# Kernel optimization log

Hardware: AMD Instinct MI355X
Metric: run time of the kernel (lower is better)

## Reference

```python
import jax, jax.numpy as jnp
import numpy as np

N, IN, H, M, D = 2048, 400, 256, 128, 8


def setup_inputs() -> dict:
    key = jax.random.key(0)
    ks = jax.random.split(key, 20)
    g = lambda k, shp, s: jax.random.normal(k, shp, jnp.float32) * s
    C = IN // 2
    return {
        "x": g(ks[0], (N, IN), 1.0),
        "memory": g(ks[1], (N, H, M), 1.0),
        "ke_w": g(ks[2], (H, C), 1.0 / np.sqrt(C)),
        "ke_b": g(ks[3], (H,), 0.01),
        "km_w": g(ks[4], (M, H), 1.0 / np.sqrt(H)),
        "km_b": g(ks[5], (M,), 0.01),
        "kw2_w": g(ks[6], (D, H), 1.0 / np.sqrt(H)),
        "kw2_b": g(ks[7], (D,), 0.01),
        "sum_w": g(ks[8], (H, 2 * H), 1.0 / np.sqrt(2 * H)),
        "sum_b": g(ks[9], (H,), 0.01),
        "out_w": g(ks[10], (1, H), 1.0 / np.sqrt(H)),
        "out_b": g(ks[11], (1,), 0.01),
        "ve_w": g(ks[12], (H, IN), 1.0 / np.sqrt(IN)),
        "ve_b": g(ks[13], (H,), 0.01),
        "er_w": g(ks[14], (D, H, H), 1.0 / np.sqrt(H)),
        "er_b": g(ks[15], (D, H), 0.01),
        "ad_w": g(ks[16], (D, H, H), 1.0 / np.sqrt(H)),
        "ad_b": g(ks[17], (D, H), 0.01),
    }


def reference(x, memory, ke_w, ke_b, km_w, km_b, kw2_w, kw2_b,
              sum_w, sum_b, out_w, out_b, ve_w, ve_b,
              er_w, er_b, ad_w, ad_b):
    n, c2 = x.shape
    c = c2 // 2
    # query = sum of the two halves of x
    q = x.reshape(n, 2, c).sum(axis=1)                       # (N, C)
    k = q @ ke_w.T + ke_b                                    # (N, H)
    w = jax.nn.softmax(k @ km_w.T + km_b, axis=-1)           # (N, M) read/write weights
    w2 = jax.nn.softmax(k @ kw2_w.T + kw2_b, axis=-1)        # (N, D) expert gates
    # memory read: weighted sum over memory slots
    r = jnp.einsum('nhm,nm->nh', memory, w)                  # (N, H)
    f = jnp.tanh(jnp.concatenate([k, r], axis=1) @ sum_w.T + sum_b)
    y = f @ out_w.T + out_b                                  # (N, 1)
    v = x @ ve_w.T + ve_b                                    # (N, H)
    # DynamicLinear: gate-weighted mixture of per-expert linear maps
    # (fused: avoids materializing per-sample (N,H,H) weights)
    e = jax.nn.sigmoid(jnp.einsum('ni,doi,nd->no', v, er_w, w2) + w2 @ er_b)
    a = jnp.tanh(jnp.einsum('ni,doi,nd->no', v, ad_w, w2) + w2 @ ad_b)
    # memory write: erase then add
    memory = memory * (1.0 - w[:, None, :] * e[:, :, None])
    memory = memory + w[:, None, :] * a[:, :, None]
    return y, memory
```

## Files before the change

### kernel.cpp

```cpp
#include <hip/hip_runtime.h>
#include <math.h>

#define N_  2048
#define IN_ 400
#define C_  200
#define H_  256
#define M_  128
#define D_  8

#define KQ   224
#define KX   416
#define KBIG 2112
#define NZ   6
#define KSPL (KBIG / NZ)
#define KS   512

typedef __bf16 bf16x8 __attribute__((ext_vector_type(8)));
typedef float  f32x4  __attribute__((ext_vector_type(4)));

__device__ __forceinline__ ushort f2bf(float x) { __bf16 b = (__bf16)x; return __builtin_bit_cast(ushort, b); }
__device__ __forceinline__ float  bf2f(ushort u) { unsigned v = ((unsigned)u) << 16; return __builtin_bit_cast(float, v); }

__device__ __forceinline__ float4 f4z() { return make_float4(0.f, 0.f, 0.f, 0.f); }
__device__ __forceinline__ float4 ld4p(const float* p, bool v) { return v ? *(const float4*)p : f4z(); }
__device__ __forceinline__ float4 add4(float4 a, float4 b) {
    return make_float4(a.x + b.x, a.y + b.y, a.z + b.z, a.w + b.w);
}
__device__ __forceinline__ uint4 pack8(float4 a, float4 b) {
    ushort u[8] = { f2bf(a.x), f2bf(a.y), f2bf(a.z), f2bf(a.w),
                    f2bf(b.x), f2bf(b.y), f2bf(b.z), f2bf(b.w) };
    return *(uint4*)u;
}

template<class F>
__device__ __forceinline__ void gemm_core(
    F&& ld, const float* __restrict__ bias,
    void* __restrict__ Cv, int ldc, int outbf,
    int m0, int n0, int kFrom, int kTo,
    ushort (*As)[128][40], ushort (*Bs)[64][40])
{
    const int tid = threadIdx.x, lane = tid & 63, wave = tid >> 6;
    const int wm = (wave >> 1) * 64, wn = (wave & 1) * 32;
    const int sr = tid >> 2, sc = (tid & 3) * 8;

    f32x4 acc[4][2] = {};

    auto compute = [&](int b) {
        const int ko = (lane >> 4) * 8;
        bf16x8 af[4], bfr[2];
#pragma unroll
        for (int i = 0; i < 4; i++)
            af[i] = __builtin_bit_cast(bf16x8, *(const uint4*)&As[b][wm + i * 16 + (lane & 15)][ko]);
#pragma unroll
        for (int j = 0; j < 2; j++)
            bfr[j] = __builtin_bit_cast(bf16x8, *(const uint4*)&Bs[b][wn + j * 16 + (lane & 15)][ko]);
#pragma unroll
        for (int i = 0; i < 4; i++)
#pragma unroll
            for (int j = 0; j < 2; j++)
                acc[i][j] = __builtin_amdgcn_mfma_f32_16x16x32_bf16(af[i], bfr[j], acc[i][j], 0, 0, 0);
    };

    uint4 a0, a1, b0;
    ld(kFrom, a0, a1, b0);
    *(uint4*)&As[0][sr][sc] = a0;
    *(uint4*)&As[0][sr + 64][sc] = a1;
    *(uint4*)&Bs[0][sr][sc] = b0;
    __syncthreads();

    int cur = 0;
    for (int k0 = kFrom + 32; k0 < kTo; k0 += 32) {
        ld(k0, a0, a1, b0);
        compute(cur);
        *(uint4*)&As[cur ^ 1][sr][sc] = a0;
        *(uint4*)&As[cur ^ 1][sr + 64][sc] = a1;
        *(uint4*)&Bs[cur ^ 1][sr][sc] = b0;
        __syncthreads();
        cur ^= 1;
    }
    compute(cur);

    float* Cf = (float*)Cv;
    ushort* Cb = (ushort*)Cv;
#pragma unroll
    for (int i = 0; i < 4; i++) {
#pragma unroll
        for (int j = 0; j < 2; j++) {
            int row = m0 + wm + i * 16 + (lane >> 4) * 4;
            int col = n0 + wn + j * 16 + (lane & 15);
#pragma unroll
            for (int r = 0; r < 4; r++) {
                float val = acc[i][j][r];
                if (bias) val += bias[col];
                if (outbf) Cb[(size_t)(row + r) * ldc + col] = f2bf(val);
                else       Cf[(size_t)(row + r) * ldc + col] = val;
            }
        }
    }
}

__global__ __launch_bounds__(256) void k1_kernel(
    const float* __restrict__ x,
    const float* __restrict__ ke_w, const float* __restrict__ ke_b, ushort* __restrict__ kr,
    const float* __restrict__ ve_w, const float* __restrict__ ve_b, float* __restrict__ v,
    const float* __restrict__ er_w, const float* __restrict__ er_b,
    const float* __restrict__ ad_w, const float* __restrict__ ad_b,
    ushort* __restrict__ wcat)
{
    __shared__ ushort As[2][128][40];
    __shared__ ushort Bs[2][64][40];
    const int z = blockIdx.z;
    const int sr = threadIdx.x >> 2, sc = (threadIdx.x & 3) * 8;

    if (z == 0) {
        const int m0 = blockIdx.y * 128, n0 = blockIdx.x * 64;
        auto ld = [&](int k0, uint4& A0, uint4& A1, uint4& B0) {
            int c0 = k0 + sc, c4 = c0 + 4;
            bool v0 = c0 < C_, v4 = c4 < C_;
            const float* r0 = x + (size_t)(m0 + sr) * IN_;
            const float* r1 = x + (size_t)(m0 + sr + 64) * IN_;
            A0 = pack8(add4(ld4p(r0 + c0, v0), ld4p(r0 + C_ + c0, v0)),
                       add4(ld4p(r0 + c4, v4), ld4p(r0 + C_ + c4, v4)));
            A1 = pack8(add4(ld4p(r1 + c0, v0), ld4p(r1 + C_ + c0, v0)),
                       add4(ld4p(r1 + c4, v4), ld4p(r1 + C_ + c4, v4)));
            const float* rb = ke_w + (size_t)(n0 + sr) * C_;
            B0 = pack8(ld4p(rb + c0, v0), ld4p(rb + c4, v4));
        };
        gemm_core(ld, ke_b, kr, KS, 1, m0, n0, 0, KQ, As, Bs);
    } else if (z == 1) {
        const int m0 = blockIdx.y * 128, n0 = blockIdx.x * 64;
        auto ld = [&](int k0, uint4& A0, uint4& A1, uint4& B0) {
            int c0 = k0 + sc, c4 = c0 + 4;
            bool v0 = c0 < IN_, v4 = c4 < IN_;
            const float* r0 = x + (size_t)(m0 + sr) * IN_;
            const float* r1 = x + (size_t)(m0 + sr + 64) * IN_;
            A0 = pack8(ld4p(r0 + c0, v0), ld4p(r0 + c4, v4));
            A1 = pack8(ld4p(r1 + c0, v0), ld4p(r1 + c4, v4));
            const float* rb = ve_w + (size_t)(n0 + sr) * IN_;
            B0 = pack8(ld4p(rb + c0, v0), ld4p(rb + c4, v4));
        };
        gemm_core(ld, ve_b, v, H_, 0, m0, n0, 0, KX, As, Bs);
    } else {
        int idx = ((z - 2) * 64 + blockIdx.y * 4 + blockIdx.x) * 256 + threadIdx.x;
        if (idx >= 512 * (KBIG / 4)) return;
        int oc = idx / (KBIG / 4), g = idx % (KBIG / 4), c0 = g * 4;
        const float* Wsrc = (oc < 256) ? er_w : ad_w;
        const float* bsrc = (oc < 256) ? er_b : ad_b;
        int oo = oc & 255;
        ushort pk[4];
#pragma unroll
        for (int j = 0; j < 4; j++) {
            int c = c0 + j;
            float val = 0.f;
            if (c < 2048)      { int d = c >> 8, ii = c & 255; val = Wsrc[(size_t)(d * 256 + oo) * 256 + ii]; }
            else if (c < 2056) { val = bsrc[(c - 2048) * 256 + oo]; }
            pk[j] = f2bf(val);
        }
        *(ushort4*)&wcat[(size_t)oc * KBIG + c0] = *(ushort4*)pk;
    }
}

__global__ __launch_bounds__(256) void vww_kernel(
    const ushort* __restrict__ kr, const float* __restrict__ v,
    const float* __restrict__ kw2_w, const float* __restrict__ kw2_b,
    const float* __restrict__ km_w, const float* __restrict__ km_b,
    float* __restrict__ wlog, ushort* __restrict__ vw)
{
    __shared__ ushort As[2][128][40];
    __shared__ ushort Bs[2][64][40];
    __shared__ float kf[H_], vl[H_], lg[8], w2l[8];
    const int b = blockIdx.x, t = threadIdx.x;
    const int sr = t >> 2, sc = (t & 3) * 8;

    if (b < 32) {
        const int m0 = (b >> 1) * 128, n0 = (b & 1) * 64;
        auto ld = [&](int k0, uint4& A0, uint4& A1, uint4& B0) {
            A0 = *(const uint4*)&kr[(size_t)(m0 + sr) * KS + k0 + sc];
            A1 = *(const uint4*)&kr[(size_t)(m0 + sr + 64) * KS + k0 + sc];
            int c0 = k0 + sc, c4 = c0 + 4;
            const float* rb = km_w + (size_t)(n0 + sr) * H_;
            B0 = pack8(*(const float4*)(rb + c0), *(const float4*)(rb + c4));
        };
        gemm_core(ld, km_b, wlog, M_, 0, m0, n0, 0, H_, As, Bs);
        return;
    }

    const int n = b - 32;
    if (t < 64) {
        ushort4 u = ((const ushort4*)(kr + (size_t)n * KS))[t];
        kf[t * 4 + 0] = bf2f(u.x); kf[t * 4 + 1] = bf2f(u.y);
        kf[t * 4 + 2] = bf2f(u.z); kf[t * 4 + 3] = bf2f(u.w);
        float4 vv = ((const float4*)(v + (size_t)n * H_))[t];
        vl[t * 4 + 0] = vv.x; vl[t * 4 + 1] = vv.y;
        vl[t * 4 + 2] = vv.z; vl[t * 4 + 3] = vv.w;
    }
    __syncthreads();
    {
        int d = t >> 5, l = t & 31;
        float acc = 0.f;
        const float* wr = kw2_w + d * H_;
#pragma unroll
        for (int s = 0; s < 8; s++) acc += kf[l + 32 * s] * wr[l + 32 * s];
#pragma unroll
        for (int off = 16; off; off >>= 1) acc += __shfl_xor(acc, off);
        if (l == 0) lg[d] = acc + kw2_b[d];
    }
    __syncthreads();
    if (t < 8) {
        float val = lg[t];
        float mx = val;
#pragma unroll
        for (int off = 1; off < 8; off <<= 1) mx = fmaxf(mx, __shfl_xor(mx, off));
        float e = expf(val - mx), s = e;
#pragma unroll
        for (int off = 1; off < 8; off <<= 1) s += __shfl_xor(s, off);
        w2l[t] = e / s;
    }
    __syncthreads();
    ushort* row = vw + (size_t)n * KBIG;
    for (int g = t; g < KBIG / 4; g += 256) {
        int c0 = g * 4;
        ushort pk[4];
#pragma unroll
        for (int j = 0; j < 4; j++) {
            int c = c0 + j;
            float val = 0.f;
            if (c < 2048)      val = w2l[c >> 8] * vl[c & 255];
            else if (c < 2056) val = w2l[c - 2048];
            pk[j] = f2bf(val);
        }
        *(ushort4*)&row[c0] = *(ushort4*)pk;
    }
}

__global__ __launch_bounds__(256) void bigw_kernel(
    const ushort* __restrict__ vw, const ushort* __restrict__ Wcat,
    float* __restrict__ parts)
{
    __shared__ ushort As[2][128][40];
    __shared__ ushort Bs[2][64][40];
    const int z = blockIdx.z;
    const int m0 = blockIdx.y * 128, n0 = blockIdx.x * 64;
    const int sr = threadIdx.x >> 2, sc = (threadIdx.x & 3) * 8;
    auto ld = [&](int k0, uint4& A0, uint4& A1, uint4& B0) {
        A0 = *(const uint4*)&vw[(size_t)(m0 + sr) * KBIG + k0 + sc];
        A1 = *(const uint4*)&vw[(size_t)(m0 + sr + 64) * KBIG + k0 + sc];
        B0 = *(const uint4*)&Wcat[(size_t)(n0 + sr) * KBIG + k0 + sc];
    };
    gemm_core(ld, nullptr, parts + (size_t)z * N_ * 512, 512, 0,
              m0, n0, z * KSPL, (z + 1) * KSPL, As, Bs);
}

__global__ __launch_bounds__(256) void mem_stream_kernel(
    const float* __restrict__ mem_in,
    const float* __restrict__ wlog,
    const float* __restrict__ parts,
    float* __restrict__ mem_out,
    ushort* __restrict__ kr)
{
    __shared__ float wl[M_];
    __shared__ float el[128], al[128];
    __shared__ float red[4];
    const int n = blockIdx.x >> 1, half = blockIdx.x & 1, hbase = half * 128;
    const int t = threadIdx.x;

    const int col = (t < 128) ? (hbase + t) : (256 + hbase + (t - 128));
    float pacc = 0.f;
#pragma unroll
    for (int z = 0; z < NZ; z++)
        pacc += parts[(size_t)z * N_ * 512 + (size_t)n * 512 + col];

    float lv = 0.f;
    if (t < 128) {
        lv = wlog[(size_t)n * M_ + t];
        float mx = lv;
#pragma unroll
        for (int off = 32; off; off >>= 1) mx = fmaxf(mx, __shfl_xor(mx, off));
        if ((t & 63) == 0) red[t >> 6] = mx;
        el[t] = 1.f / (1.f + expf(-pacc));
    } else {
        al[t - 128] = tanhf(pacc);
    }
    __syncthreads();
    if (t < 128) {
        float gmax = fmaxf(red[0], red[1]);
        float ev = expf(lv - gmax);
        float s = ev;
#pragma unroll
        for (int off = 32; off; off >>= 1) s += __shfl_xor(s, off);
        if ((t & 63) == 0) red[2 + (t >> 6)] = s;
        wl[t] = ev;
    }
    __syncthreads();
    if (t < 128) wl[t] *= 1.f / (red[2] + red[3]);
    __syncthreads();

    const int wave = t >> 6, lane = t & 63, half2 = lane >> 5, l32 = lane & 31;
    const int hrow = wave * 2 + half2;
    const f32x4* min4 = (const f32x4*)(mem_in + ((size_t)n * H_ + hbase) * M_);
    f32x4* mout4 = (f32x4*)(mem_out + ((size_t)n * H_ + hbase) * M_);
    f32x4 wv = ((const f32x4*)wl)[l32];

    float racc[16];
    float eh[16], ah[16];
#pragma unroll
    for (int i = 0; i < 16; i++) { eh[i] = el[i * 8 + hrow]; ah[i] = al[i * 8 + hrow]; }
#pragma unroll
    for (int i = 0; i < 16; i++) {
        f32x4 mv = __builtin_nontemporal_load(&min4[(i * 8 + hrow) * 32 + l32]);
        f32x4 nv = mv * (1.f - wv * eh[i]) + wv * ah[i];
        __builtin_nontemporal_store(nv, &mout4[(i * 8 + hrow) * 32 + l32]);
        racc[i] = mv[0] * wv[0] + mv[1] * wv[1] + mv[2] * wv[2] + mv[3] * wv[3];
    }

#pragma unroll
    for (int i = 0; i < 16; i++) {
        float r = racc[i];
#pragma unroll
        for (int off = 1; off < 32; off <<= 1) r += __shfl_xor(r, off);
        if (l32 == 0) kr[(size_t)n * KS + H_ + hbase + i * 8 + hrow] = f2bf(r);
    }
}

__global__ __launch_bounds__(256) void fy_kernel(
    const ushort* __restrict__ kr, const float* __restrict__ sum_w,
    const float* __restrict__ sum_b, const float* __restrict__ out_w,
    const float* __restrict__ out_b, float* __restrict__ y)
{
    __shared__ ushort As[2][64][40];
    __shared__ ushort Bs[2][256][40];
    __shared__ float yl[64][4];
    const int tid = threadIdx.x, lane = tid & 63, wave = tid >> 6;
    const int wn = wave * 64;
    const int m0 = blockIdx.x * 64;
    const int sr = tid >> 2, sc = (tid & 3) * 8;

    f32x4 acc[4][4] = {};

    auto compute = [&](int b) {
        const int ko = (lane >> 4) * 8;
        bf16x8 af[4], bfr[4];
#pragma unroll
        for (int i = 0; i < 4; i++)
            af[i] = __builtin_bit_cast(bf16x8, *(const uint4*)&As[b][i * 16 + (lane & 15)][ko]);
#pragma unroll
        for (int j = 0; j < 4; j++)
            bfr[j] = __builtin_bit_cast(bf16x8, *(const uint4*)&Bs[b][wn + j * 16 + (lane & 15)][ko]);
#pragma unroll
        for (int i = 0; i < 4; i++)
#pragma unroll
            for (int j = 0; j < 4; j++)
                acc[i][j] = __builtin_amdgcn_mfma_f32_16x16x32_bf16(af[i], bfr[j], acc[i][j], 0, 0, 0);
    };

    auto stage = [&](int buf, int k0) {
        int c0 = k0 + sc, c4 = c0 + 4;
        *(uint4*)&As[buf][sr][sc] = *(const uint4*)&kr[(size_t)(m0 + sr) * KS + k0 + sc];
#pragma unroll
        for (int g = 0; g < 4; g++) {
            const float* rb = sum_w + (size_t)(sr + g * 64) * KS;
            *(uint4*)&Bs[buf][sr + g * 64][sc] = pack8(*(const float4*)(rb + c0), *(const float4*)(rb + c4));
        }
    };

    stage(0, 0);
    __syncthreads();
    int cur = 0;
    for (int k0 = 32; k0 < KS; k0 += 32) {
        compute(cur);
        stage(cur ^ 1, k0);
        __syncthreads();
        cur ^= 1;
    }
    compute(cur);

    float ow[4], sb[4];
#pragma unroll
    for (int j = 0; j < 4; j++) {
        int col = wn + j * 16 + (lane & 15);
        ow[j] = out_w[col];
        sb[j] = sum_b[col];
    }
    float yp[4][4];
#pragma unroll
    for (int i = 0; i < 4; i++)
#pragma unroll
        for (int r = 0; r < 4; r++) {
            float s = 0.f;
#pragma unroll
            for (int j = 0; j < 4; j++)
                s += tanhf(acc[i][j][r] + sb[j]) * ow[j];
            yp[i][r] = s;
        }
#pragma unroll
    for (int off = 1; off < 16; off <<= 1)
#pragma unroll
        for (int i = 0; i < 4; i++)
#pragma unroll
            for (int r = 0; r < 4; r++)
                yp[i][r] += __shfl_xor(yp[i][r], off);
    if ((lane & 15) == 0) {
#pragma unroll
        for (int i = 0; i < 4; i++)
#pragma unroll
            for (int r = 0; r < 4; r++)
                yl[i * 16 + (lane >> 4) * 4 + r][wave] = yp[i][r];
    }
    __syncthreads();
    if (tid < 64)
        y[m0 + tid] = yl[tid][0] + yl[tid][1] + yl[tid][2] + yl[tid][3] + out_b[0];
}

extern "C" void kernel_launch(void* const* d_in, const int* in_sizes, int n_in,
                              void* d_out, int out_size, void* d_ws, size_t ws_size,
                              hipStream_t stream) {
    const float* x      = (const float*)d_in[0];
    const float* mem_in = (const float*)d_in[1];
    const float* ke_w   = (const float*)d_in[2];
    const float* ke_b   = (const float*)d_in[3];
    const float* km_w   = (const float*)d_in[4];
    const float* km_b   = (const float*)d_in[5];
    const float* kw2_w  = (const float*)d_in[6];
    const float* kw2_b  = (const float*)d_in[7];
    const float* sum_w  = (const float*)d_in[8];
    const float* sum_b  = (const float*)d_in[9];
    const float* out_w  = (const float*)d_in[10];
    const float* out_b  = (const float*)d_in[11];
    const float* ve_w   = (const float*)d_in[12];
    const float* ve_b   = (const float*)d_in[13];
    const float* er_w   = (const float*)d_in[14];
    const float* er_b   = (const float*)d_in[15];
    const float* ad_w   = (const float*)d_in[16];
    const float* ad_b   = (const float*)d_in[17];

    float* y_out   = (float*)d_out;
    float* mem_out = (float*)d_out + N_;

    float* ws = (float*)d_ws;
    size_t o = 0;
    float*  parts = ws + o;            o += (size_t)NZ * N_ * 512;
    ushort* vw    = (ushort*)(ws + o); o += (size_t)N_ * KBIG / 2;
    ushort* Wcat  = (ushort*)(ws + o); o += (size_t)512 * KBIG / 2;
    ushort* kr    = (ushort*)(ws + o); o += (size_t)N_ * KS / 2;
    float*  v     = ws + o;            o += (size_t)N_ * H_;
    float*  wlog  = ws + o;            o += (size_t)N_ * M_;

    k1_kernel<<<dim3(4, 16, 19), 256, 0, stream>>>(
        x, ke_w, ke_b, kr, ve_w, ve_b, v, er_w, er_b, ad_w, ad_b, Wcat);
    vww_kernel<<<32 + N_, 256, 0, stream>>>(
        kr, v, kw2_w, kw2_b, km_w, km_b, wlog, vw);
    bigw_kernel<<<dim3(8, 16, NZ), 256, 0, stream>>>(vw, Wcat, parts);
    mem_stream_kernel<<<2 * N_, 256, 0, stream>>>(mem_in, wlog, parts, mem_out, kr);
    fy_kernel<<<N_ / 64, 256, 0, stream>>>(kr, sum_w, sum_b, out_w, out_b, y_out);
}
```

Measured before the change: 174.6 us.

## Restructure memory stream kernel to two samples per block with software-pipelined loads

```diff
diff --git a/kernel.cpp b/kernel.cpp
--- a/kernel.cpp
+++ b/kernel.cpp
@@ -258,67 +258,87 @@
     float* __restrict__ mem_out,
     ushort* __restrict__ kr)
 {
-    __shared__ float wl[M_];
-    __shared__ float el[128], al[128];
-    __shared__ float red[4];
-    const int n = blockIdx.x >> 1, half = blockIdx.x & 1, hbase = half * 128;
+    __shared__ float wl2[2][M_];
+    __shared__ float el2[2][H_], al2[2][H_];
+    __shared__ float red[2][4];
+    const int n0 = blockIdx.x * 2;
     const int t = threadIdx.x;
 
-    const int col = (t < 128) ? (hbase + t) : (256 + hbase + (t - 128));
-    float pacc = 0.f;
-#pragma unroll
-    for (int z = 0; z < NZ; z++)
-        pacc += parts[(size_t)z * N_ * 512 + (size_t)n * 512 + col];
-
-    float lv = 0.f;
-    if (t < 128) {
-        lv = wlog[(size_t)n * M_ + t];
+#pragma unroll
+    for (int it = 0; it < 4; it++) {
+        int idx = it * 256 + t;
+        int rep = idx >> 9, cc = idx & 511;
+        float pacc = 0.f;
+#pragma unroll
+        for (int z = 0; z < NZ; z++)
+            pacc += parts[(size_t)z * N_ * 512 + (size_t)(n0 + rep) * 512 + cc];
+        if (cc < 256) el2[rep][cc] = 1.f / (1.f + expf(-pacc));
+        else          al2[rep][cc - 256] = tanhf(pacc);
+    }
+
+    {
+        const int pair = t >> 7, tp = t & 127, wip = (t >> 6) & 1;
+        float lv = wlog[(size_t)(n0 + pair) * M_ + tp];
         float mx = lv;
 #pragma unroll
         for (int off = 32; off; off >>= 1) mx = fmaxf(mx, __shfl_xor(mx, off));
-        if ((t & 63) == 0) red[t >> 6] = mx;
-        el[t] = 1.f / (1.f + expf(-pacc));
-    } else {
-        al[t - 128] = tanhf(pacc);
-    }
-    __syncthreads();
-    if (t < 128) {
-        float gmax = fmaxf(red[0], red[1]);
+        if ((t & 63) == 0) red[pair][wip] = mx;
+        __syncthreads();
+        float gmax = fmaxf(red[pair][0], red[pair][1]);
         float ev = expf(lv - gmax);
         float s = ev;
 #pragma unroll
         for (int off = 32; off; off >>= 1) s += __shfl_xor(s, off);
-        if ((t & 63) == 0) red[2 + (t >> 6)] = s;
-        wl[t] = ev;
-    }
-    __syncthreads();
-    if (t < 128) wl[t] *= 1.f / (red[2] + red[3]);
+        if ((t & 63) == 0) red[pair][2 + wip] = s;
+        __syncthreads();
+        wl2[pair][tp] = ev / (red[pair][2] + red[pair][3]);
+    }
     __syncthreads();
 
     const int wave = t >> 6, lane = t & 63, half2 = lane >> 5, l32 = lane & 31;
     const int hrow = wave * 2 + half2;
-    const f32x4* min4 = (const f32x4*)(mem_in + ((size_t)n * H_ + hbase) * M_);
-    f32x4* mout4 = (f32x4*)(mem_out + ((size_t)n * H_ + hbase) * M_);
-    f32x4 wv = ((const f32x4*)wl)[l32];
-
-    float racc[16];
-    float eh[16], ah[16];
-#pragma unroll
-    for (int i = 0; i < 16; i++) { eh[i] = el[i * 8 + hrow]; ah[i] = al[i * 8 + hrow]; }
-#pragma unroll
-    for (int i = 0; i < 16; i++) {
-        f32x4 mv = __builtin_nontemporal_load(&min4[(i * 8 + hrow) * 32 + l32]);
-        f32x4 nv = mv * (1.f - wv * eh[i]) + wv * ah[i];
-        __builtin_nontemporal_store(nv, &mout4[(i * 8 + hrow) * 32 + l32]);
-        racc[i] = mv[0] * wv[0] + mv[1] * wv[1] + mv[2] * wv[2] + mv[3] * wv[3];
-    }
-
-#pragma unroll
-    for (int i = 0; i < 16; i++) {
-        float r = racc[i];
-#pragma unroll
-        for (int off = 1; off < 32; off <<= 1) r += __shfl_xor(r, off);
-        if (l32 == 0) kr[(size_t)n * KS + H_ + hbase + i * 8 + hrow] = f2bf(r);
+
+#pragma unroll
+    for (int rep = 0; rep < 2; rep++) {
+        const int n = n0 + rep;
+        const f32x4* min4 = (const f32x4*)(mem_in + (size_t)n * H_ * M_);
+        f32x4* mout4 = (f32x4*)(mem_out + (size_t)n * H_ * M_);
+        f32x4 wv = ((const f32x4*)wl2[rep])[l32];
+
+        f32x4 mv[2][4];
+#pragma unroll
+        for (int j = 0; j < 4; j++)
+            mv[0][j] = __builtin_nontemporal_load(&min4[(j * 8 + hrow) * 32 + l32]);
+
+#pragma unroll
+        for (int c = 0; c < 8; c++) {
+            if (c < 7) {
+#pragma unroll
+                for (int j = 0; j < 4; j++)
+                    mv[(c + 1) & 1][j] = __builtin_nontemporal_load(
+                        &min4[(((c + 1) * 4 + j) * 8 + hrow) * 32 + l32]);
+            }
+            __builtin_amdgcn_sched_barrier(0);
+            float racc[4];
+#pragma unroll
+            for (int j = 0; j < 4; j++) {
+                int row = (c * 4 + j) * 8 + hrow;
+                f32x4 m = mv[c & 1][j];
+                float eh = el2[rep][row], ah = al2[rep][row];
+                f32x4 nv = m * (1.f - wv * eh) + wv * ah;
+                mout4[row * 32 + l32] = nv;
+                racc[j] = m[0] * wv[0] + m[1] * wv[1] + m[2] * wv[2] + m[3] * wv[3];
+            }
+#pragma unroll
+            for (int j = 0; j < 4; j++) {
+                float r = racc[j];
+#pragma unroll
+                for (int off = 1; off < 32; off <<= 1) r += __shfl_xor(r, off);
+                if (l32 == 0)
+                    kr[(size_t)n * KS + H_ + (c * 4 + j) * 8 + hrow] = f2bf(r);
+            }
+            __builtin_amdgcn_sched_barrier(0);
+        }
     }
 }
 
@@ -450,6 +470,6 @@
     vww_kernel<<<32 + N_, 256, 0, stream>>>(
         kr, v, kw2_w, kw2_b, km_w, km_b, wlog, vw);
     bigw_kernel<<<dim3(8, 16, NZ), 256, 0, stream>>>(vw, Wcat, parts);
-    mem_stream_kernel<<<2 * N_, 256, 0, stream>>>(mem_in, wlog, parts, mem_out, kr);
+    mem_stream_kernel<<<N_ / 2, 256, 0, stream>>>(mem_in, wlog, parts, mem_out, kr);
     fy_kernel<<<N_ / 64, 256, 0, stream>>>(kr, sum_w, sum_b, out_w, out_b, y_out);
 }
```

After: 175.1 us. No clear change (+0.3%).

## Stream memory tiles through LDS with async global_load_lds in quarter-row blocks

Applied to the files above, without the earlier changes.

```diff
diff --git a/kernel.cpp b/kernel.cpp
--- a/kernel.cpp
+++ b/kernel.cpp
@@ -17,6 +17,9 @@
 
 typedef __bf16 bf16x8 __attribute__((ext_vector_type(8)));
 typedef float  f32x4  __attribute__((ext_vector_type(4)));
+
+typedef const __attribute__((address_space(1))) unsigned int* gas_t;
+typedef __attribute__((address_space(3))) unsigned int* las_t;
 
 __device__ __forceinline__ ushort f2bf(float x) { __bf16 b = (__bf16)x; return __builtin_bit_cast(ushort, b); }
 __device__ __forceinline__ float  bf2f(ushort u) { unsigned v = ((unsigned)u) << 16; return __builtin_bit_cast(float, v); }
@@ -258,67 +261,82 @@
     float* __restrict__ mem_out,
     ushort* __restrict__ kr)
 {
+    __shared__ float ring[4][2048];
     __shared__ float wl[M_];
-    __shared__ float el[128], al[128];
+    __shared__ float el[64], al[64];
     __shared__ float red[4];
-    const int n = blockIdx.x >> 1, half = blockIdx.x & 1, hbase = half * 128;
+    const int n = blockIdx.x >> 2, q = blockIdx.x & 3, hbase = q * 64;
     const int t = threadIdx.x;
-
-    const int col = (t < 128) ? (hbase + t) : (256 + hbase + (t - 128));
-    float pacc = 0.f;
-#pragma unroll
-    for (int z = 0; z < NZ; z++)
-        pacc += parts[(size_t)z * N_ * 512 + (size_t)n * 512 + col];
 
     float lv = 0.f;
     if (t < 128) {
-        lv = wlog[(size_t)n * M_ + t];
+        int isA = t >> 6, tt = t & 63;
+        int col = isA * 256 + hbase + tt;
+        float pacc = 0.f;
+#pragma unroll
+        for (int z = 0; z < NZ; z++)
+            pacc += parts[(size_t)z * N_ * 512 + (size_t)n * 512 + col];
+        if (isA) al[tt] = tanhf(pacc);
+        else     el[tt] = 1.f / (1.f + expf(-pacc));
+    } else {
+        int tt = t - 128;
+        lv = wlog[(size_t)n * M_ + tt];
         float mx = lv;
 #pragma unroll
         for (int off = 32; off; off >>= 1) mx = fmaxf(mx, __shfl_xor(mx, off));
-        if ((t & 63) == 0) red[t >> 6] = mx;
-        el[t] = 1.f / (1.f + expf(-pacc));
-    } else {
-        al[t - 128] = tanhf(pacc);
-    }
-    __syncthreads();
-    if (t < 128) {
+        if ((t & 63) == 0) red[(t >> 6) - 2] = mx;
+    }
+    __syncthreads();
+    if (t >= 128) {
+        int tt = t - 128;
         float gmax = fmaxf(red[0], red[1]);
         float ev = expf(lv - gmax);
         float s = ev;
 #pragma unroll
         for (int off = 32; off; off >>= 1) s += __shfl_xor(s, off);
-        if ((t & 63) == 0) red[2 + (t >> 6)] = s;
-        wl[t] = ev;
-    }
-    __syncthreads();
-    if (t < 128) wl[t] *= 1.f / (red[2] + red[3]);
-    __syncthreads();
-
-    const int wave = t >> 6, lane = t & 63, half2 = lane >> 5, l32 = lane & 31;
-    const int hrow = wave * 2 + half2;
-    const f32x4* min4 = (const f32x4*)(mem_in + ((size_t)n * H_ + hbase) * M_);
-    f32x4* mout4 = (f32x4*)(mem_out + ((size_t)n * H_ + hbase) * M_);
+        if ((t & 63) == 0) red[2 + (t >> 6) - 2] = s;
+        wl[tt] = ev;
+    }
+    __syncthreads();
+    if (t >= 128) wl[t - 128] *= 1.f / (red[2] + red[3]);
+    __syncthreads();
+
+    const int wave = t >> 6, lane = t & 63;
+    const int l32 = lane & 31, hi = lane >> 5;
+    const int rowg0 = hbase + wave * 16;
+    const float* gsrc = mem_in + ((size_t)n * H_ + rowg0) * M_;
+    float* gdst = mem_out + ((size_t)n * H_ + rowg0) * M_;
+    float* lbase = ring[wave];
+
+#pragma unroll
+    for (int c = 0; c < 8; c++) {
+        __builtin_amdgcn_global_load_lds(
+            (gas_t)(const void*)(gsrc + c * 256 + lane * 4),
+            (las_t)(void*)(lbase + c * 256),
+            16, 0, 0);
+    }
+
     f32x4 wv = ((const f32x4*)wl)[l32];
-
-    float racc[16];
-    float eh[16], ah[16];
-#pragma unroll
-    for (int i = 0; i < 16; i++) { eh[i] = el[i * 8 + hrow]; ah[i] = al[i * 8 + hrow]; }
-#pragma unroll
-    for (int i = 0; i < 16; i++) {
-        f32x4 mv = __builtin_nontemporal_load(&min4[(i * 8 + hrow) * 32 + l32]);
-        f32x4 nv = mv * (1.f - wv * eh[i]) + wv * ah[i];
-        __builtin_nontemporal_store(nv, &mout4[(i * 8 + hrow) * 32 + l32]);
-        racc[i] = mv[0] * wv[0] + mv[1] * wv[1] + mv[2] * wv[2] + mv[3] * wv[3];
-    }
-
-#pragma unroll
-    for (int i = 0; i < 16; i++) {
-        float r = racc[i];
+    float racc[8];
+#pragma unroll
+    for (int c = 0; c < 8; c++) {
+        asm volatile("s_waitcnt vmcnt(7)" ::: "memory");
+        __builtin_amdgcn_sched_barrier(0);
+        f32x4 mv = *(const f32x4*)&lbase[c * 256 + lane * 4];
+        int rloc = c * 2 + hi;
+        float eh = el[wave * 16 + rloc], ah = al[wave * 16 + rloc];
+        f32x4 nv = mv * (1.f - wv * eh) + wv * ah;
+        __builtin_nontemporal_store(nv, (f32x4*)(gdst + c * 256 + lane * 4));
+        racc[c] = mv[0] * wv[0] + mv[1] * wv[1] + mv[2] * wv[2] + mv[3] * wv[3];
+    }
+
+#pragma unroll
+    for (int c = 0; c < 8; c++) {
+        float r = racc[c];
 #pragma unroll
         for (int off = 1; off < 32; off <<= 1) r += __shfl_xor(r, off);
-        if (l32 == 0) kr[(size_t)n * KS + H_ + hbase + i * 8 + hrow] = f2bf(r);
+        if (l32 == 0)
+            kr[(size_t)n * KS + H_ + rowg0 + c * 2 + hi] = f2bf(r);
     }
 }
 
@@ -450,6 +468,6 @@
     vww_kernel<<<32 + N_, 256, 0, stream>>>(
         kr, v, kw2_w, kw2_b, km_w, km_b, wlog, vw);
     bigw_kernel<<<dim3(8, 16, NZ), 256, 0, stream>>>(vw, Wcat, parts);
-    mem_stream_kernel<<<2 * N_, 256, 0, stream>>>(mem_in, wlog, parts, mem_out, kr);
+    mem_stream_kernel<<<4 * N_, 256, 0, stream>>>(mem_in, wlog, parts, mem_out, kr);
     fy_kernel<<<N_ / 64, 256, 0, stream>>>(kr, sum_w, sum_b, out_w, out_b, y_out);
 }
```

New measurement: 167.4 us. -4.1%, faster.
